# Kernel optimization log

Hardware: AMD Instinct MI355X
Metric: run time of the kernel (lower is better)

Reference implementation:

```python
import jax, jax.numpy as jnp
import numpy as np

D, H, L, FF, IN, OUT, S, B = 512, 8, 6, 2048, 32, 3, 512, 32


def setup_inputs() -> dict:
    key = jax.random.key(0)
    ks = iter(jax.random.split(key, 32))
    w = lambda shape: jax.random.normal(next(ks), shape, jnp.float32) * 0.02
    z = lambda shape: jnp.zeros(shape, jnp.float32)
    o = lambda shape: jnp.ones(shape, jnp.float32)
    return {
        'x': jax.random.normal(next(ks), (B, S, IN), jnp.float32),
        'w_in': w((IN, D)), 'b_in': z((D,)), 'g_in': o((D,)), 'be_in': z((D,)),
        'w_qkv': w((L, D, 3 * D)), 'b_qkv': z((L, 3 * D)),
        'w_out': w((L, D, D)), 'b_out': z((L, D)),
        'g1': o((L, D)), 'be1': z((L, D)),
        'w_ff1': w((L, D, FF)), 'b_ff1': z((L, FF)),
        'w_ff2': w((L, FF, D)), 'b_ff2': z((L, D)),
        'g2': o((L, D)), 'be2': z((L, D)),
        'w_h1': w((D, D // 2)), 'b_h1': z((D // 2,)),
        'w_h2': w((D // 2, OUT)), 'b_h2': z((OUT,)),
    }


def _layer_norm(x, g, b, eps=1e-5):
    mu = jnp.mean(x, axis=-1, keepdims=True)
    var = jnp.mean(jnp.square(x - mu), axis=-1, keepdims=True)
    return (x - mu) / jnp.sqrt(var + eps) * g + b


def _gelu(x):
    return jax.nn.gelu(x, approximate=False)  # torch nn.GELU default (erf)


def _pos_encoding(seq_len, d_model):
    pos = jnp.arange(seq_len, dtype=jnp.float32)[:, None]
    div = jnp.exp(jnp.arange(0, d_model, 2, dtype=jnp.float32) * (-np.log(10000.0) / d_model))
    pe = jnp.zeros((seq_len, d_model), jnp.float32)
    pe = pe.at[:, 0::2].set(jnp.sin(pos * div))
    pe = pe.at[:, 1::2].set(jnp.cos(pos * div))
    return pe


def reference(x, w_in, b_in, g_in, be_in, w_qkv, b_qkv, w_out, b_out,
              g1, be1, w_ff1, b_ff1, w_ff2, b_ff2, g2, be2,
              w_h1, b_h1, w_h2, b_h2):
    b, s, _ = x.shape
    d = w_in.shape[1]
    hd = d // H
    scale = hd ** -0.5

    # input projection: Linear -> LayerNorm -> GELU (dropout = identity at eval)
    h = _gelu(_layer_norm(x @ w_in + b_in, g_in, be_in))
    h = h + _pos_encoding(s, d)

    causal_mask = jnp.triu(jnp.ones((s, s), bool), 1)  # True above diagonal = future

    for l in range(w_qkv.shape[0]):
        qkv = (h @ w_qkv[l] + b_qkv[l]).reshape(b, s, 3, H, hd)
        q, k, v = qkv[:, :, 0], qkv[:, :, 1], qkv[:, :, 2]  # [b, s, H, hd]
        scores = jnp.einsum('bihd,bjhd->bhij', q, k) * scale
        scores = jnp.where(causal_mask, -jnp.inf, scores)
        attn = jax.nn.softmax(scores, axis=-1)
        o = jnp.einsum('bhij,bjhd->bihd', attn, v).reshape(b, s, d)
        o = o @ w_out[l] + b_out[l]
        h = _layer_norm(h + o, g1[l], be1[l])
        f = _gelu(h @ w_ff1[l] + b_ff1[l]) @ w_ff2[l] + b_ff2[l]
        h = _layer_norm(h + f, g2[l], be2[l])

    logits = _gelu(h @ w_h1 + b_h1) @ w_h2 + b_h2  # [b, s, OUT]
    return logits[:, -1, :]  # last position only
```

## Files before the change

kernel.cpp:

```cpp
#include <hip/hip_runtime.h>
#include <hip/hip_bf16.h>
#include <math.h>

#define D_   512
#define H_   8
#define HD_  64
#define L_   6
#define FF_  2048
#define IN_  32
#define OUT_ 3
#define S_   512
#define B_   32
#define M_   (B_ * S_)

typedef __attribute__((ext_vector_type(8))) short short8;
typedef __attribute__((ext_vector_type(4))) float floatx4;

__device__ __forceinline__ float gelu_f(float x) {
    return 0.5f * x * (1.0f + erff(x * 0.7071067811865475f));
}
__device__ __forceinline__ float bf2f(unsigned short u) {
    union { unsigned int i; float f; } c; c.i = ((unsigned)u) << 16; return c.f;
}
__device__ __forceinline__ unsigned short f2bf(float v) {
    __hip_bfloat16 t = __float2bfloat16(v);
    return *(unsigned short*)&t;
}
__device__ __forceinline__ void async16(const void* g, void* l) {
    __builtin_amdgcn_global_load_lds(
        (const __attribute__((address_space(1))) unsigned int*)g,
        (__attribute__((address_space(3))) unsigned int*)l, 16, 0, 0);
}

template<int DO_GELU, int OUT_BF16, int ADD_RES>
__global__ __launch_bounds__(256)
void gemm_mfma_k(const __hip_bfloat16* __restrict__ A,
                 const __hip_bfloat16* __restrict__ WT,
                 const float* __restrict__ bias,
                 const float* __restrict__ R,
                 void* __restrict__ C,
                 int N, int K) {
    __shared__ __align__(16) char smem[34816];
    short* As0 = (short*)(smem);
    short* As1 = (short*)(smem + 8192);
    short* Bs0 = (short*)(smem + 16384);
    short* Bs1 = (short*)(smem + 24576);
    float* Ep  = (float*)smem;

    const int tid  = threadIdx.x;
    const int lane = tid & 63;
    const int wave = tid >> 6;

    const int Lid = blockIdx.y * gridDim.x + blockIdx.x;
    const int xcd = Lid & 7;
    const int idx = Lid >> 3;
    const int gx  = gridDim.x, gy8 = gridDim.y >> 3;
    const int m0 = (xcd * gy8 + idx / gx) * 128;
    const int n0 = (idx % gx) * 128;

    const int wm = (wave >> 1) * 64, wn = (wave & 1) * 64;

    const int srow = tid >> 2;
    const int scol = ((tid & 3) ^ (srow & 3)) * 8;
    const short* Ag = (const short*)A + (long)(m0 + srow) * K + scol;
    const short* Bg = (const short*)WT + (long)(n0 + srow) * K + scol;

    floatx4 acc[4][4];
    #pragma unroll
    for (int i = 0; i < 4; i++)
        #pragma unroll
        for (int j = 0; j < 4; j++) acc[i][j] = (floatx4)0.f;

    const int r = lane & 15, q = lane >> 4;
    const int qa = (q ^ (r & 3)) * 8;

    for (int k0 = 0; k0 < K; k0 += 64) {
        async16(Ag + k0,                     As0 + tid * 8);
        async16(Ag + (long)64 * K + k0,      As0 + 2048 + tid * 8);
        async16(Ag + k0 + 32,                As1 + tid * 8);
        async16(Ag + (long)64 * K + k0 + 32, As1 + 2048 + tid * 8);
        async16(Bg + k0,                     Bs0 + tid * 8);
        async16(Bg + (long)64 * K + k0,      Bs0 + 2048 + tid * 8);
        async16(Bg + k0 + 32,                Bs1 + tid * 8);
        async16(Bg + (long)64 * K + k0 + 32, Bs1 + 2048 + tid * 8);
        __syncthreads();

        #pragma unroll
        for (int c = 0; c < 2; c++) {
            const short* Asc = c ? As1 : As0;
            const short* Bsc = c ? Bs1 : Bs0;
            short8 af[4], bf[4];
            #pragma unroll
            for (int t = 0; t < 4; t++)
                af[t] = *(const short8*)&Asc[(wm + t * 16 + r) * 32 + qa];
            #pragma unroll
            for (int t = 0; t < 4; t++)
                bf[t] = *(const short8*)&Bsc[(wn + t * 16 + r) * 32 + qa];
            #pragma unroll
            for (int i = 0; i < 4; i++)
                #pragma unroll
                for (int j = 0; j < 4; j++)
                    acc[i][j] = __builtin_amdgcn_mfma_f32_16x16x32_bf16(
                        af[i], bf[j], acc[i][j], 0, 0, 0);
        }
        __syncthreads();
    }

    const int erow = tid >> 5;
    const int ecol = (tid & 31) * 4;
    const float4 bvec = *(const float4*)&bias[n0 + ecol];

    #pragma unroll
    for (int pass = 0; pass < 2; pass++) {
        if (pass) __syncthreads();
        if ((wave >> 1) == pass) {
            #pragma unroll
            for (int i = 0; i < 4; i++)
                #pragma unroll
                for (int j = 0; j < 4; j++)
                    #pragma unroll
                    for (int rg = 0; rg < 4; rg++)
                        Ep[(i * 16 + q * 4 + rg) * 132 + wn + j * 16 + r] =
                            acc[i][j][rg];
        }
        __syncthreads();
        #pragma unroll
        for (int it = 0; it < 8; it++) {
            const int row = it * 8 + erow;
            const long grow = (long)(m0 + pass * 64 + row) * N + n0 + ecol;
            const float4 v = *(const float4*)&Ep[row * 132 + ecol];
            float o0 = v.x + bvec.x, o1 = v.y + bvec.y;
            float o2 = v.z + bvec.z, o3 = v.w + bvec.w;
            if (DO_GELU) {
                o0 = gelu_f(o0); o1 = gelu_f(o1);
                o2 = gelu_f(o2); o3 = gelu_f(o3);
            }
            if (ADD_RES) {
                const float4 rv = *(const float4*)&R[grow];
                o0 += rv.x; o1 += rv.y; o2 += rv.z; o3 += rv.w;
            }
            if (OUT_BF16) {
                ushort4 pk;
                pk.x = f2bf(o0); pk.y = f2bf(o1);
                pk.z = f2bf(o2); pk.w = f2bf(o3);
                *(ushort4*)((unsigned short*)C + grow) = pk;
            } else {
                *(float4*)((float*)C + grow) = make_float4(o0, o1, o2, o3);
            }
        }
    }
}

__global__ __launch_bounds__(256)
void transpose_cast_k(const float* __restrict__ W, __hip_bfloat16* __restrict__ WT,
                      int K, int N) {
    __shared__ float tile[32][33];
    const float* Wl = W + (long)blockIdx.z * K * N;
    __hip_bfloat16* WTl = WT + (long)blockIdx.z * K * N;
    const int n0 = blockIdx.x * 32, k0 = blockIdx.y * 32;
    const int tx = threadIdx.x & 31, ty = threadIdx.x >> 5;
    for (int rr = ty; rr < 32; rr += 8)
        tile[rr][tx] = Wl[(long)(k0 + rr) * N + n0 + tx];
    __syncthreads();
    for (int rr = ty; rr < 32; rr += 8)
        WTl[(long)(n0 + rr) * K + k0 + tx] = __float2bfloat16(tile[tx][rr]);
}

template<int DO_GELU>
__global__ __launch_bounds__(256)
void gemm_bias_k(const float* __restrict__ A, long lda,
                 const float* __restrict__ W,
                 const float* __restrict__ bias,
                 float* __restrict__ C,
                 int M, int N, int K) {
    __shared__ float As[16][64];
    __shared__ float Ws[16][64];
    const int tx = threadIdx.x;
    const int ty = threadIdx.y;
    const int tid = ty * 16 + tx;
    const int m0 = blockIdx.y * 64;
    const int n0 = blockIdx.x * 64;
    float acc[4][4] = {};
    for (int k0 = 0; k0 < K; k0 += 16) {
        #pragma unroll
        for (int e = tid; e < 64 * 16; e += 256) {
            int m = e >> 4, k = e & 15;
            float v = 0.f;
            if (m0 + m < M) v = A[(long)(m0 + m) * lda + k0 + k];
            As[k][m] = v;
        }
        #pragma unroll
        for (int e = tid; e < 16 * 64; e += 256) {
            int k = e >> 6, n = e & 63;
            float v = 0.f;
            if (n0 + n < N) v = W[(long)(k0 + k) * N + n0 + n];
            Ws[k][n] = v;
        }
        __syncthreads();
        #pragma unroll
        for (int kk = 0; kk < 16; kk++) {
            float a[4], w[4];
            #pragma unroll
            for (int i = 0; i < 4; i++) a[i] = As[kk][ty * 4 + i];
            #pragma unroll
            for (int j = 0; j < 4; j++) w[j] = Ws[kk][tx * 4 + j];
            #pragma unroll
            for (int i = 0; i < 4; i++)
                #pragma unroll
                for (int j = 0; j < 4; j++)
                    acc[i][j] += a[i] * w[j];
        }
        __syncthreads();
    }
    #pragma unroll
    for (int i = 0; i < 4; i++) {
        int m = m0 + ty * 4 + i;
        if (m >= M) continue;
        #pragma unroll
        for (int j = 0; j < 4; j++) {
            int n = n0 + tx * 4 + j;
            if (n >= N) continue;
            float v = acc[i][j] + bias[n];
            if (DO_GELU) v = gelu_f(v);
            C[(long)m * N + n] = v;
        }
    }
}

__global__ __launch_bounds__(256)
void ln_k(const float* __restrict__ X,
          const float* __restrict__ g,
          const float* __restrict__ be,
          float* __restrict__ H,
          __hip_bfloat16* __restrict__ Hb) {
    const int row = blockIdx.x * 4 + (threadIdx.x >> 6);
    const int lane = threadIdx.x & 63;
    const float* xp = X + (long)row * D_ + lane * 8;
    const float4 a = *(const float4*)xp;
    const float4 c = *(const float4*)(xp + 4);
    float s = a.x + a.y + a.z + a.w + c.x + c.y + c.z + c.w;
    #pragma unroll
    for (int off = 1; off < 64; off <<= 1) s += __shfl_xor(s, off);
    const float mu = s * (1.0f / D_);
    float d[8] = { a.x - mu, a.y - mu, a.z - mu, a.w - mu,
                   c.x - mu, c.y - mu, c.z - mu, c.w - mu };
    float ss = 0.f;
    #pragma unroll
    for (int e = 0; e < 8; e++) ss += d[e] * d[e];
    #pragma unroll
    for (int off = 1; off < 64; off <<= 1) ss += __shfl_xor(ss, off);
    const float inv = 1.0f / sqrtf(ss * (1.0f / D_) + 1e-5f);
    const float4 g0 = *(const float4*)(g + lane * 8);
    const float4 g1 = *(const float4*)(g + lane * 8 + 4);
    const float4 e0 = *(const float4*)(be + lane * 8);
    const float4 e1 = *(const float4*)(be + lane * 8 + 4);
    const float gv[8] = { g0.x, g0.y, g0.z, g0.w, g1.x, g1.y, g1.z, g1.w };
    const float ev[8] = { e0.x, e0.y, e0.z, e0.w, e1.x, e1.y, e1.z, e1.w };
    float o[8];
    short8 pk;
    #pragma unroll
    for (int e = 0; e < 8; e++) {
        o[e] = d[e] * inv * gv[e] + ev[e];
        pk[e] = (short)f2bf(o[e]);
    }
    float* hp = H + (long)row * D_ + lane * 8;
    *(float4*)hp = make_float4(o[0], o[1], o[2], o[3]);
    *(float4*)(hp + 4) = make_float4(o[4], o[5], o[6], o[7]);
    *(short8*)((unsigned short*)Hb + (long)row * D_ + lane * 8) = pk;
}

__global__ __launch_bounds__(256)
void ln_gelu_pos_k(const float* __restrict__ X,
                   const float* __restrict__ g,
                   const float* __restrict__ be,
                   float* __restrict__ Hout,
                   __hip_bfloat16* __restrict__ Hb) {
    const int row = blockIdx.x;
    const int s = row & (S_ - 1);
    const int t = threadIdx.x;
    const float* x = X + (long)row * D_;
    float v0 = x[t], v1 = x[t + 256];
    __shared__ float red[256];
    red[t] = v0 + v1;
    __syncthreads();
    for (int off = 128; off; off >>= 1) {
        if (t < off) red[t] += red[t + off];
        __syncthreads();
    }
    float mu = red[0] * (1.0f / D_);
    __syncthreads();
    float d0 = v0 - mu, d1 = v1 - mu;
    red[t] = d0 * d0 + d1 * d1;
    __syncthreads();
    for (int off = 128; off; off >>= 1) {
        if (t < off) red[t] += red[t + off];
        __syncthreads();
    }
    float var = red[0] * (1.0f / D_);
    float inv = 1.0f / sqrtf(var + 1e-5f);
    float o0 = gelu_f(d0 * inv * g[t] + be[t]);
    float o1 = gelu_f(d1 * inv * g[t + 256] + be[t + 256]);
    {
        int d = t, i = d >> 1;
        float dv = expf((float)(2 * i) * (-9.210340371976184f / 512.0f));
        float ang = (float)s * dv;
        o0 += (d & 1) ? cosf(ang) : sinf(ang);
    }
    {
        int d = t + 256, i = d >> 1;
        float dv = expf((float)(2 * i) * (-9.210340371976184f / 512.0f));
        float ang = (float)s * dv;
        o1 += (d & 1) ? cosf(ang) : sinf(ang);
    }
    Hout[(long)row * D_ + t] = o0;
    Hout[(long)row * D_ + t + 256] = o1;
    Hb[(long)row * D_ + t] = __float2bfloat16(o0);
    Hb[(long)row * D_ + t + 256] = __float2bfloat16(o1);
}

#define LDT 72
__global__ __launch_bounds__(256)
void attn_mfma_k(const __hip_bfloat16* __restrict__ qkv,
                 __hip_bfloat16* __restrict__ O) {
    const int qt = blockIdx.x;
    const int bh = blockIdx.y;
    const int b = bh >> 3, h = bh & (H_ - 1);
    const int tid = threadIdx.x;
    const int wave = tid >> 6, lane = tid & 63;
    const int ln = lane & 15, quad = lane >> 4;
    const int wm = wave * 32;
    const int i0 = qt * 128;

    __shared__ unsigned short Qs[128 * LDT];
    __shared__ unsigned short Ks[64 * LDT];
    __shared__ unsigned short Vt[64 * LDT];
    __shared__ unsigned short Ps[128 * LDT];
    __shared__ float stat[128];

    const unsigned short* base = (const unsigned short*)qkv + (long)b * S_ * (3 * D_);

    {
        const int r0 = tid >> 3, c0 = (tid & 7) * 8;
        #pragma unroll
        for (int i = 0; i < 4; i++) {
            const int rw = i * 32 + r0;
            *(short8*)&Qs[rw * LDT + c0] =
                *(const short8*)(base + (long)(i0 + rw) * (3 * D_) + h * HD_ + c0);
        }
    }

    float m_i[2] = { -INFINITY, -INFINITY };
    float l_i[2] = { 0.f, 0.f };
    floatx4 o_acc[2][4];
    #pragma unroll
    for (int i = 0; i < 2; i++)
        #pragma unroll
        for (int j = 0; j < 4; j++) o_acc[i][j] = (floatx4)0.f;

    const int kr = tid >> 2, kc = (tid & 3) * 16;
    const int vj = tid & 63, vc = (tid >> 6) * 16;

    const int ktmax = 2 * qt + 1;
    for (int kt = 0; kt <= ktmax; kt++) {
        const int j0 = kt * 64;
        {
            const unsigned short* kp = base + (long)(j0 + kr) * (3 * D_) + D_ + h * HD_ + kc;
            *(short8*)&Ks[kr * LDT + kc]     = *(const short8*)(kp);
            *(short8*)&Ks[kr * LDT + kc + 8] = *(const short8*)(kp + 8);
            const unsigned short* vp = base + (long)(j0 + vj) * (3 * D_) + 2 * D_ + h * HD_ + vc;
            short8 v0 = *(const short8*)(vp);
            short8 v1 = *(const short8*)(vp + 8);
            #pragma unroll
            for (int e = 0; e < 8; e++) {
                Vt[(vc + e) * LDT + vj]     = (unsigned short)v0[e];
                Vt[(vc + 8 + e) * LDT + vj] = (unsigned short)v1[e];
            }
        }
        __syncthreads();

        floatx4 sa[4][2];
        #pragma unroll
        for (int mt = 0; mt < 4; mt++)
            #pragma unroll
            for (int nt = 0; nt < 2; nt++) sa[mt][nt] = (floatx4)0.f;
        #pragma unroll
        for (int c = 0; c < 2; c++) {
            short8 kf[4], qf[2];
            #pragma unroll
            for (int mt = 0; mt < 4; mt++)
                kf[mt] = *(const short8*)&Ks[(mt * 16 + ln) * LDT + c * 32 + quad * 8];
            #pragma unroll
            for (int nt = 0; nt < 2; nt++)
                qf[nt] = *(const short8*)&Qs[(wm + nt * 16 + ln) * LDT + c * 32 + quad * 8];
            #pragma unroll
            for (int mt = 0; mt < 4; mt++)
                #pragma unroll
                for (int nt = 0; nt < 2; nt++)
                    sa[mt][nt] = __builtin_amdgcn_mfma_f32_16x16x32_bf16(
                        kf[mt], qf[nt], sa[mt][nt], 0, 0, 0);
        }

        const bool domask = (kt >= 2 * qt);
        #pragma unroll
        for (int nt = 0; nt < 2; nt++) {
            const int qg = i0 + wm + nt * 16 + ln;
            float mx = -INFINITY;
            #pragma unroll
            for (int mt = 0; mt < 4; mt++)
                #pragma unroll
                for (int rg = 0; rg < 4; rg++) {
                    float v = sa[mt][nt][rg] * 0.125f;
                    if (domask && (j0 + mt * 16 + quad * 4 + rg > qg)) v = -INFINITY;
                    sa[mt][nt][rg] = v;
                    mx = fmaxf(mx, v);
                }
            mx = fmaxf(mx, __shfl_xor(mx, 16));
            mx = fmaxf(mx, __shfl_xor(mx, 32));
            const float mn = fmaxf(m_i[nt], mx);
            const float alpha = __expf(m_i[nt] - mn);
            m_i[nt] = mn;
            float ls = 0.f;
            #pragma unroll
            for (int mt = 0; mt < 4; mt++) {
                ushort4 pk;
                float p0 = __expf(sa[mt][nt][0] - mn);
                float p1 = __expf(sa[mt][nt][1] - mn);
                float p2 = __expf(sa[mt][nt][2] - mn);
                float p3 = __expf(sa[mt][nt][3] - mn);
                ls += p0 + p1 + p2 + p3;
                pk.x = f2bf(p0); pk.y = f2bf(p1); pk.z = f2bf(p2); pk.w = f2bf(p3);
                *(ushort4*)&Ps[(wm + nt * 16 + ln) * LDT + mt * 16 + quad * 4] = pk;
            }
            ls += __shfl_xor(ls, 16);
            ls += __shfl_xor(ls, 32);
            l_i[nt] = l_i[nt] * alpha + ls;
            if (quad == 0) stat[wm + nt * 16 + ln] = alpha;
        }

        #pragma unroll
        for (int mt2 = 0; mt2 < 2; mt2++) {
            #pragma unroll
            for (int rg = 0; rg < 4; rg++) {
                const float a = stat[wm + mt2 * 16 + quad * 4 + rg];
                #pragma unroll
                for (int nt = 0; nt < 4; nt++) o_acc[mt2][nt][rg] *= a;
            }
        }

        #pragma unroll
        for (int c = 0; c < 2; c++) {
            short8 pf[2], vf[4];
            #pragma unroll
            for (int mt2 = 0; mt2 < 2; mt2++)
                pf[mt2] = *(const short8*)&Ps[(wm + mt2 * 16 + ln) * LDT + c * 32 + quad * 8];
            #pragma unroll
            for (int nt = 0; nt < 4; nt++)
                vf[nt] = *(const short8*)&Vt[(nt * 16 + ln) * LDT + c * 32 + quad * 8];
            #pragma unroll
            for (int mt2 = 0; mt2 < 2; mt2++)
                #pragma unroll
                for (int nt = 0; nt < 4; nt++)
                    o_acc[mt2][nt] = __builtin_amdgcn_mfma_f32_16x16x32_bf16(
                        pf[mt2], vf[nt], o_acc[mt2][nt], 0, 0, 0);
        }
        __syncthreads();
    }

    if (quad == 0) {
        stat[wm + ln]      = l_i[0];
        stat[wm + 16 + ln] = l_i[1];
    }
    unsigned short* Og = (unsigned short*)O;
    #pragma unroll
    for (int mt2 = 0; mt2 < 2; mt2++) {
        #pragma unroll
        for (int rg = 0; rg < 4; rg++) {
            const float linv = 1.0f / stat[wm + mt2 * 16 + quad * 4 + rg];
            const long row = (long)(b * S_ + i0 + wm + mt2 * 16 + quad * 4 + rg);
            #pragma unroll
            for (int nt = 0; nt < 4; nt++)
                Og[row * D_ + h * HD_ + nt * 16 + ln] =
                    f2bf(o_acc[mt2][nt][rg] * linv);
        }
    }
}

__global__ __launch_bounds__(256)
void head1_k(const float* __restrict__ h, const float* __restrict__ w1,
             const float* __restrict__ b1, float* __restrict__ th) {
    __shared__ float hs[D_];
    const int b = blockIdx.x, n = threadIdx.x;
    const float* hr = h + (long)(b * S_ + S_ - 1) * D_;
    hs[n] = hr[n];
    hs[n + 256] = hr[n + 256];
    __syncthreads();
    float s = 0.f;
    #pragma unroll 8
    for (int k = 0; k < D_; k++) s += hs[k] * w1[(long)k * 256 + n];
    th[b * 256 + n] = gelu_f(s + b1[n]);
}

__global__ __launch_bounds__(64)
void head2_k(const float* __restrict__ th, const float* __restrict__ w2,
             const float* __restrict__ b2, float* __restrict__ out) {
    const int b = blockIdx.x, lane = threadIdx.x;
    const float* t = th + b * 256;
    float s0 = 0.f, s1 = 0.f, s2 = 0.f;
    #pragma unroll
    for (int e = 0; e < 4; e++) {
        const int k = lane * 4 + e;
        const float tv = t[k];
        s0 += tv * w2[k * 3 + 0];
        s1 += tv * w2[k * 3 + 1];
        s2 += tv * w2[k * 3 + 2];
    }
    #pragma unroll
    for (int off = 1; off < 64; off <<= 1) {
        s0 += __shfl_xor(s0, off);
        s1 += __shfl_xor(s1, off);
        s2 += __shfl_xor(s2, off);
    }
    if (lane == 0) {
        out[b * 3 + 0] = s0 + b2[0];
        out[b * 3 + 1] = s1 + b2[1];
        out[b * 3 + 2] = s2 + b2[2];
    }
}

extern "C" void kernel_launch(void* const* d_in, const int* in_sizes, int n_in,
                              void* d_out, int out_size, void* d_ws, size_t ws_size,
                              hipStream_t stream) {
    const float* x     = (const float*)d_in[0];
    const float* w_in  = (const float*)d_in[1];
    const float* b_in  = (const float*)d_in[2];
    const float* g_in  = (const float*)d_in[3];
    const float* be_in = (const float*)d_in[4];
    const float* w_qkv = (const float*)d_in[5];
    const float* b_qkv = (const float*)d_in[6];
    const float* w_out = (const float*)d_in[7];
    const float* b_out = (const float*)d_in[8];
    const float* g1    = (const float*)d_in[9];
    const float* be1   = (const float*)d_in[10];
    const float* w_ff1 = (const float*)d_in[11];
    const float* b_ff1 = (const float*)d_in[12];
    const float* w_ff2 = (const float*)d_in[13];
    const float* b_ff2 = (const float*)d_in[14];
    const float* g2    = (const float*)d_in[15];
    const float* be2   = (const float*)d_in[16];
    const float* w_h1  = (const float*)d_in[17];
    const float* b_h1  = (const float*)d_in[18];
    const float* w_h2  = (const float*)d_in[19];
    const float* b_h2  = (const float*)d_in[20];
    float* out = (float*)d_out;

    float* h    = (float*)d_ws;
    float* bufB = h + (long)M_ * D_;
    float* th   = bufB + (long)M_ * D_;
    __hip_bfloat16* hb    = (__hip_bfloat16*)(th + 32 * 256);
    __hip_bfloat16* attb  = hb + (long)M_ * D_;
    __hip_bfloat16* bufAb = attb + (long)M_ * D_;
    __hip_bfloat16* qkvT  = bufAb + (long)M_ * FF_;
    __hip_bfloat16* outT  = qkvT + (long)L_ * (3 * D_) * D_;
    __hip_bfloat16* ff1T  = outT + (long)L_ * D_ * D_;
    __hip_bfloat16* ff2T  = ff1T + (long)L_ * FF_ * D_;

    dim3 blk(16, 16);

    transpose_cast_k<<<dim3((3 * D_) / 32, D_ / 32, L_), 256, 0, stream>>>(w_qkv, qkvT, D_, 3 * D_);
    transpose_cast_k<<<dim3(D_ / 32, D_ / 32, L_), 256, 0, stream>>>(w_out, outT, D_, D_);
    transpose_cast_k<<<dim3(FF_ / 32, D_ / 32, L_), 256, 0, stream>>>(w_ff1, ff1T, D_, FF_);
    transpose_cast_k<<<dim3(D_ / 32, FF_ / 32, L_), 256, 0, stream>>>(w_ff2, ff2T, FF_, D_);

    gemm_bias_k<0><<<dim3(D_ / 64, M_ / 64), blk, 0, stream>>>(
        x, IN_, w_in, b_in, bufB, M_, D_, IN_);
    ln_gelu_pos_k<<<M_, 256, 0, stream>>>(bufB, g_in, be_in, h, hb);

    for (int l = 0; l < L_; l++) {
        gemm_mfma_k<0, 1, 0><<<dim3((3 * D_) / 128, M_ / 128), 256, 0, stream>>>(
            hb, qkvT + (long)l * (3 * D_) * D_, b_qkv + l * 3 * D_, nullptr,
            bufAb, 3 * D_, D_);
        attn_mfma_k<<<dim3(S_ / 128, B_ * H_), 256, 0, stream>>>(bufAb, attb);
        gemm_mfma_k<0, 0, 1><<<dim3(D_ / 128, M_ / 128), 256, 0, stream>>>(
            attb, outT + (long)l * D_ * D_, b_out + l * D_, h,
            bufB, D_, D_);
        ln_k<<<M_ / 4, 256, 0, stream>>>(bufB, g1 + l * D_, be1 + l * D_, h, hb);
        gemm_mfma_k<1, 1, 0><<<dim3(FF_ / 128, M_ / 128), 256, 0, stream>>>(
            hb, ff1T + (long)l * FF_ * D_, b_ff1 + l * FF_, nullptr,
            bufAb, FF_, D_);
        gemm_mfma_k<0, 0, 1><<<dim3(D_ / 128, M_ / 128), 256, 0, stream>>>(
            bufAb, ff2T + (long)l * D_ * FF_, b_ff2 + l * D_, h,
            bufB, D_, FF_);
        ln_k<<<M_ / 4, 256, 0, stream>>>(bufB, g2 + l * D_, be2 + l * D_, h, hb);
    }

    head1_k<<<B_, 256, 0, stream>>>(h, w_h1, b_h1, th);
    head2_k<<<B_, 64, 0, stream>>>(th, w_h2, b_h2, out);
}
```

Measured before the change: 1.736 ms.

## Double-buffer GEMM LDS tiles to overlap global loads with MFMA compute

The GEMM K-loop now uses two LDS stages. The next 64-wide K tile is fetched asynchronously while MFMAs run on the current one, which also cuts the loop from two barriers per iteration to one. The aim is to hide global-to-LDS load latency behind compute. In exchange, LDS per block grows from 34 KB to 64 KB, which may lower occupancy. It also relies on the barrier ordering correctly with the async LDS writes, since there is no explicit vmcnt wait before the barrier.

```diff
diff --git a/kernel.cpp b/kernel.cpp
--- a/kernel.cpp
+++ b/kernel.cpp
@@ -40,12 +40,8 @@
                  const float* __restrict__ R,
                  void* __restrict__ C,
                  int N, int K) {
-    __shared__ __align__(16) char smem[34816];
-    short* As0 = (short*)(smem);
-    short* As1 = (short*)(smem + 8192);
-    short* Bs0 = (short*)(smem + 16384);
-    short* Bs1 = (short*)(smem + 24576);
-    float* Ep  = (float*)smem;
+    __shared__ __align__(16) char smem[65536];
+    float* Ep = (float*)smem;
 
     const int tid  = threadIdx.x;
     const int lane = tid & 63;
@@ -74,21 +70,44 @@
     const int r = lane & 15, q = lane >> 4;
     const int qa = (q ^ (r & 3)) * 8;
 
-    for (int k0 = 0; k0 < K; k0 += 64) {
-        async16(Ag + k0,                     As0 + tid * 8);
-        async16(Ag + (long)64 * K + k0,      As0 + 2048 + tid * 8);
-        async16(Ag + k0 + 32,                As1 + tid * 8);
-        async16(Ag + (long)64 * K + k0 + 32, As1 + 2048 + tid * 8);
-        async16(Bg + k0,                     Bs0 + tid * 8);
-        async16(Bg + (long)64 * K + k0,      Bs0 + 2048 + tid * 8);
-        async16(Bg + k0 + 32,                Bs1 + tid * 8);
-        async16(Bg + (long)64 * K + k0 + 32, Bs1 + 2048 + tid * 8);
-        __syncthreads();
-
+    const int nIter = K >> 6;
+
+    {
+        short* As_ = (short*)smem;
+        short* Bs_ = (short*)(smem + 16384);
+        async16(Ag,                     As_ + tid * 8);
+        async16(Ag + (long)64 * K,      As_ + 2048 + tid * 8);
+        async16(Ag + 32,                As_ + 4096 + tid * 8);
+        async16(Ag + (long)64 * K + 32, As_ + 6144 + tid * 8);
+        async16(Bg,                     Bs_ + tid * 8);
+        async16(Bg + (long)64 * K,      Bs_ + 2048 + tid * 8);
+        async16(Bg + 32,                Bs_ + 4096 + tid * 8);
+        async16(Bg + (long)64 * K + 32, Bs_ + 6144 + tid * 8);
+    }
+
+    for (int i = 0; i < nIter; i++) {
+        __syncthreads();
+
+        if (i + 1 < nIter) {
+            const int k0 = (i + 1) << 6;
+            short* As_ = (short*)(smem + ((i + 1) & 1) * 32768);
+            short* Bs_ = (short*)(smem + ((i + 1) & 1) * 32768 + 16384);
+            async16(Ag + k0,                     As_ + tid * 8);
+            async16(Ag + (long)64 * K + k0,      As_ + 2048 + tid * 8);
+            async16(Ag + k0 + 32,                As_ + 4096 + tid * 8);
+            async16(Ag + (long)64 * K + k0 + 32, As_ + 6144 + tid * 8);
+            async16(Bg + k0,                     Bs_ + tid * 8);
+            async16(Bg + (long)64 * K + k0,      Bs_ + 2048 + tid * 8);
+            async16(Bg + k0 + 32,                Bs_ + 4096 + tid * 8);
+            async16(Bg + (long)64 * K + k0 + 32, Bs_ + 6144 + tid * 8);
+        }
+
+        const short* As_ = (const short*)(smem + (i & 1) * 32768);
+        const short* Bs_ = (const short*)(smem + (i & 1) * 32768 + 16384);
         #pragma unroll
         for (int c = 0; c < 2; c++) {
-            const short* Asc = c ? As1 : As0;
-            const short* Bsc = c ? Bs1 : Bs0;
+            const short* Asc = As_ + c * 4096;
+            const short* Bsc = Bs_ + c * 4096;
             short8 af[4], bf[4];
             #pragma unroll
             for (int t = 0; t < 4; t++)
@@ -97,14 +116,14 @@
             for (int t = 0; t < 4; t++)
                 bf[t] = *(const short8*)&Bsc[(wn + t * 16 + r) * 32 + qa];
             #pragma unroll
-            for (int i = 0; i < 4; i++)
+            for (int i2 = 0; i2 < 4; i2++)
                 #pragma unroll
                 for (int j = 0; j < 4; j++)
-                    acc[i][j] = __builtin_amdgcn_mfma_f32_16x16x32_bf16(
-                        af[i], bf[j], acc[i][j], 0, 0, 0);
-        }
-        __syncthreads();
-    }
+                    acc[i2][j] = __builtin_amdgcn_mfma_f32_16x16x32_bf16(
+                        af[i2], bf[j], acc[i2][j], 0, 0, 0);
+        }
+    }
+    __syncthreads();
 
     const int erow = tid >> 5;
     const int ecol = (tid & 31) * 4;
```

New measurement: 1.683 ms. -3.0%, faster.
